# Performance work log

Measured on AMD Instinct MI355X. Metric: run time of the kernel, lower is better.

The kernel has to match this reference:

```python
import jax, jax.numpy as jnp
import numpy as np

D, E, DFF, TOPK = 768, 4, 1024, 2


def setup_inputs() -> dict:
    key = jax.random.key(0)
    ks = jax.random.split(key, 6)
    s = 0.02  # init scale for weights
    return {
        "input_ids": jax.random.normal(ks[0], (8, 2048, D), dtype=jnp.float32),
        "W": jax.random.normal(ks[1], (D, D), dtype=jnp.float32) * s,
        "b": jnp.zeros((D,), dtype=jnp.float32),
        "Wg": jax.random.normal(ks[2], (D, E), dtype=jnp.float32) * s,
        "bg": jnp.zeros((E,), dtype=jnp.float32),
        "W1": jax.random.normal(ks[3], (E, D, DFF), dtype=jnp.float32) * s,
        "b1": jnp.zeros((E, DFF), dtype=jnp.float32),
        "W2": jax.random.normal(ks[4], (E, DFF, D), dtype=jnp.float32) * s,
        "b2": jnp.zeros((E, D), dtype=jnp.float32),
    }


def reference(input_ids, W, b, Wg, bg, W1, b1, W2, b2):
    B, S, _ = input_ids.shape
    # Dense projection feeding the MoE layer
    h = jnp.einsum("bsd,de->bse", input_ids, W) + b          # [B,S,D]
    t = h.reshape(-1, D)                                      # [T,D] tokens

    # Token-choice router: softmax over experts, top-2, renormalized gates
    logits = t @ Wg + bg                                      # [T,E]
    probs = jax.nn.softmax(logits, axis=-1)
    vals, idx = jax.lax.top_k(probs, TOPK)                    # [T,K]
    gates = vals / jnp.sum(vals, axis=-1, keepdims=True)
    # Dense combine weights [T,E]: zero for non-selected experts
    comb = jnp.sum(jax.nn.one_hot(idx, E, dtype=t.dtype) * gates[..., None], axis=1)

    # Expert FFNs (E small -> compute all experts, weighted combine)
    pre = jnp.einsum("td,edf->etf", t, W1) + b1[:, None, :]   # [E,T,DFF]
    y_e = jnp.einsum("etf,efd->etd", jax.nn.gelu(pre), W2) + b2[:, None, :]
    out = jnp.einsum("te,etd->td", comb, y_e)                 # [T,D]
    return out.reshape(B, S, D)
```

## Files before the change

### kernel.cpp

```cpp
#include <hip/hip_runtime.h>

#define DIM 768
#define NEXP 4
#define DFF_ 1024
#define CAP 16384

typedef __attribute__((ext_vector_type(4))) float f32x4;
typedef __attribute__((ext_vector_type(8))) short s16x8;

__device__ __forceinline__ unsigned short f32_to_bf16(float f) {
  unsigned int u = __float_as_uint(f);
  unsigned int r = (u + 0x7FFFu + ((u >> 16) & 1u)) >> 16;
  return (unsigned short)r;
}
__device__ __forceinline__ float bf16_to_f32(unsigned short u) {
  return __uint_as_float(((unsigned int)u) << 16);
}
__device__ __forceinline__ unsigned lds_off(const void* p) {
  return (unsigned)(unsigned long long)(__attribute__((address_space(3))) const void*)p;
}

__global__ void pack_bf16_kernel(const float* __restrict__ in,
                                 unsigned short* __restrict__ out,
                                 int K, int C) {
  const int t = threadIdx.x;
  const int lane = t & 63;
  const int pb = blockIdx.x * 4 + (t >> 6);
  const int KT = K >> 5;
  const int n16 = pb / KT, kt = pb - n16 * KT;
  const int z = blockIdx.z;
  in  += (size_t)z * K * C;
  out += (size_t)z * K * C;
  const int col = n16 * 16 + (lane & 15);
  const int k0 = kt * 32 + (lane >> 4) * 8;
  s16x8 vv;
#pragma unroll
  for (int e = 0; e < 8; e++) vv[e] = (short)f32_to_bf16(in[(size_t)(k0 + e) * C + col]);
  *(s16x8*)(out + (size_t)pb * 512 + lane * 8) = vv;
}

__global__ void wfg_kernel(const float* __restrict__ W, const float* __restrict__ Wg,
                           const float* __restrict__ b, const float* __restrict__ bg,
                           float* __restrict__ wfg, float* __restrict__ bgp) {
  int gid = blockIdx.x * 256 + threadIdx.x;
  if (gid < DIM * NEXP) {
    int k = gid >> 2, e = gid & 3;
    const float* wr = W + (size_t)k * DIM;
    float acc = 0.f;
    for (int d = 0; d < DIM; d++) acc += wr[d] * Wg[d * NEXP + e];
    wfg[gid] = acc;
  } else if (gid < DIM * NEXP + NEXP) {
    int e = gid - DIM * NEXP;
    float acc = bg[e];
    for (int d = 0; d < DIM; d++) acc += b[d] * Wg[d * NEXP + e];
    bgp[e] = acc;
  }
}

__global__ void router_kernel(const float* __restrict__ x, const float* __restrict__ wfg,
                              const float* __restrict__ bgp,
                              int2* __restrict__ rte, float2* __restrict__ rtg,
                              unsigned short* __restrict__ xbf) {
  __shared__ float wfgS[DIM * NEXP];
  const int tid = threadIdx.x;
  for (int i = tid; i < DIM * NEXP; i += 256) wfgS[i] = wfg[i];
  __syncthreads();
  const int w = tid >> 6, lane = tid & 63;
  const size_t t = (size_t)blockIdx.x * 4 + w;
  const float* xr = x + t * DIM;
  unsigned short* xbr = xbf + t * DIM;
  float a0 = 0.f, a1 = 0.f, a2 = 0.f, a3 = 0.f;
#pragma unroll
  for (int i = 0; i < 6; i++) {
    int k = i * 128 + lane * 2;
    float2 xv = *(const float2*)(xr + k);
    ushort2 pk;
    pk.x = f32_to_bf16(xv.x);
    pk.y = f32_to_bf16(xv.y);
    *(ushort2*)(xbr + k) = pk;
    a0 += xv.x * wfgS[k * 4 + 0] + xv.y * wfgS[k * 4 + 4];
    a1 += xv.x * wfgS[k * 4 + 1] + xv.y * wfgS[k * 4 + 5];
    a2 += xv.x * wfgS[k * 4 + 2] + xv.y * wfgS[k * 4 + 6];
    a3 += xv.x * wfgS[k * 4 + 3] + xv.y * wfgS[k * 4 + 7];
  }
#pragma unroll
  for (int off = 32; off > 0; off >>= 1) {
    a0 += __shfl_xor(a0, off);
    a1 += __shfl_xor(a1, off);
    a2 += __shfl_xor(a2, off);
    a3 += __shfl_xor(a3, off);
  }
  if (lane == 0) {
    float l[NEXP] = {a0 + bgp[0], a1 + bgp[1], a2 + bgp[2], a3 + bgp[3]};
    float m = fmaxf(fmaxf(l[0], l[1]), fmaxf(l[2], l[3]));
    float p[NEXP]; float s = 0.f;
#pragma unroll
    for (int e = 0; e < NEXP; e++) { p[e] = expf(l[e] - m); s += p[e]; }
#pragma unroll
    for (int e = 0; e < NEXP; e++) p[e] /= s;
    int i1 = 0;
#pragma unroll
    for (int e = 1; e < NEXP; e++) if (p[e] > p[i1]) i1 = e;
    int i2 = -1;
#pragma unroll
    for (int e = 0; e < NEXP; e++) { if (e == i1) continue; if (i2 < 0 || p[e] > p[i2]) i2 = e; }
    float denom = p[i1] + p[i2];
    rte[t] = make_int2(i1, i2);
    rtg[t] = make_float2(p[i1] / denom, p[i2] / denom);
  }
}

__global__ void assign_kernel(const int2* __restrict__ rte, const float2* __restrict__ rtg,
                              int* __restrict__ cnt, int* __restrict__ idx_tok,
                              float* __restrict__ gate_sel, int2* __restrict__ tok_slot) {
  __shared__ int hist[NEXP];
  __shared__ int base[NEXP];
  const int tid = threadIdx.x;
  if (tid < NEXP) hist[tid] = 0;
  __syncthreads();
  const int t = blockIdx.x * 256 + tid;
  int2 e = rte[t];
  float2 g = rtg[t];
  int r1 = atomicAdd(&hist[e.x], 1);
  int r2 = atomicAdd(&hist[e.y], 1);
  __syncthreads();
  if (tid < NEXP) base[tid] = atomicAdd(&cnt[tid], hist[tid]);
  __syncthreads();
  int s1 = base[e.x] + r1, s2 = base[e.y] + r2;
  idx_tok[e.x * CAP + s1] = t;  gate_sel[e.x * CAP + s1] = g.x;
  idx_tok[e.y * CAP + s2] = t;  gate_sel[e.y * CAP + s2] = g.y;
  tok_slot[t] = make_int2((e.x << 14) | s1, (e.y << 14) | s2);
}

__global__ void combine_kernel(const unsigned short* __restrict__ y,
                               const int2* __restrict__ tok_slot,
                               const float2* __restrict__ rtg,
                               const int* __restrict__ cnts,
                               const float* __restrict__ b2,
                               float* __restrict__ out) {
  __shared__ float b2S[NEXP * DIM];
  const int tid = threadIdx.x;
  for (int i = tid; i < NEXP * DIM; i += 256) b2S[i] = b2[i];
  const int t0 = (cnts[0] + 127) >> 7, t1 = (cnts[1] + 127) >> 7, t2 = (cnts[2] + 127) >> 7;
  const int rb[NEXP] = {0, t0 * 128, (t0 + t1) * 128, (t0 + t1 + t2) * 128};
  __syncthreads();
  const int w = tid >> 6, lane = tid & 63;
  const size_t t = (size_t)blockIdx.x * 4 + w;
  int2 v = tok_slot[t];
  float2 cg = rtg[t];
  const int e1 = v.x >> 14, s1 = v.x & (CAP - 1);
  const int e2 = v.y >> 14, s2 = v.y & (CAP - 1);
  const unsigned short* y1 = y + (size_t)(rb[e1] + s1) * DIM;
  const unsigned short* y2 = y + (size_t)(rb[e2] + s2) * DIM;
  float* op = out + t * DIM;
  const float* bp1 = b2S + e1 * DIM;
  const float* bp2 = b2S + e2 * DIM;
#pragma unroll
  for (int k = 0; k < 12; k++) {
    int n = k * 64 + lane;
    op[n] = bf16_to_f32(y1[n]) + bf16_to_f32(y2[n]) + cg.x * bp1[n] + cg.y * bp2[n];
  }
}

template <int MODE, int CH, int NT>
__launch_bounds__(256, 3)
__global__ void gemm_kernel(const unsigned short* __restrict__ A, const int lda,
                            const unsigned short* __restrict__ Bp, const int ldb,
                            const int N,
                            const float* __restrict__ bias,
                            const int* __restrict__ idx_tok,
                            const float* __restrict__ gate_sel,
                            const int* __restrict__ cnts,
                            unsigned short* __restrict__ outB, const int ldo) {
  const int lin = blockIdx.y * gridDim.x + blockIdx.x;
  const int nT = gridDim.x;
  const int xcd = lin & 7, t8 = lin >> 3;
  int bn = 0, bm0 = 0;
  int bmLoc = 0, cnt = 1 << 30, segBase = 0, gRow0 = 0;
  const unsigned short* Bt = Bp;

  if constexpr (MODE == 0) {
    const int perXcd = gridDim.y >> 3;
    const int mi = t8 % CH;
    const int rest = t8 / CH;
    bn = rest % nT;
    const int mc = rest / nT;
    bm0 = (xcd * perXcd + mc * CH + mi) * 128;
  } else {
    const int c0 = cnts[0], c1 = cnts[1], c2 = cnts[2], c3 = cnts[3];
    const int t0 = (c0 + 127) >> 7, t1 = (c1 + 127) >> 7,
              t2 = (c2 + 127) >> 7, t3 = (c3 + 127) >> 7;
    const int p1 = t0, p2 = p1 + t1, p3 = p2 + t2, tot = p3 + t3;
    const int perXcd = (tot + 7) >> 3;
    bn = t8 % nT;
    const int mloc = t8 / nT;
    if (mloc >= perXcd) return;
    const int mIdx = xcd * perXcd + mloc;
    if (mIdx >= tot) return;
    const int seg = (mIdx >= p2) ? ((mIdx >= p3) ? 3 : 2) : ((mIdx >= p1) ? 1 : 0);
    const int pre = (seg == 3) ? p3 : (seg == 2) ? p2 : (seg == 1) ? p1 : 0;
    bmLoc = (mIdx - pre) * 128;
    segBase = seg * CAP;
    gRow0 = mIdx * 128;
    cnt = (seg == 3) ? c3 : (seg == 2) ? c2 : (seg == 1) ? c1 : c0;
    Bt += (size_t)seg * N * ldb;
    if constexpr (MODE == 1) bias += (size_t)seg * N;
  }

  __shared__ unsigned short As[4][3][2048];
  __shared__ int idxS[128];
  __shared__ float gateS[128];

  const int tid = threadIdx.x;
  const int w = tid >> 6;
  const int lane = tid & 63;

  if constexpr (MODE == 1) {
    if (tid < 128) {
      int r = bmLoc + tid;
      int cl = (r < cnt) ? r : bmLoc;
      idxS[tid] = idx_tok[segBase + cl];
      gateS[tid] = gate_sel[segBase + cl];
    }
    __syncthreads();
  }

  const int quad = lane >> 4;
  const int m16 = lane & 15;
  const int wm = (w & 1) * 64;
  const int wn = (w >> 1) * 64;

  const int lrow = lane >> 2;
  const int lslot = (lane & 3) ^ (lrow & 3);
  const unsigned short* aSrc[4];
#pragma unroll
  for (int q = 0; q < 4; q++) {
    const int rw = q * 16 + lrow;
    size_t grow;
    if constexpr (MODE == 0) grow = (size_t)(bm0 + wm + rw);
    else if constexpr (MODE == 1) grow = (size_t)idxS[wm + rw];
    else grow = (size_t)(gRow0 + wm + rw);
    aSrc[q] = A + grow * lda + lslot * 8;
  }

  const unsigned wBase = lds_off(&As[w][0][0]);
  const unsigned aRd = (unsigned)(m16 * 64 + ((quad ^ (m16 & 3)) * 16));
  const unsigned aAd0 = wBase + aRd;
  const unsigned aAd1 = wBase + 4096u + aRd;
  const unsigned aAd2 = wBase + 8192u + aRd;

  const unsigned short* bq0 = Bt + (size_t)(bn * 8 + (w >> 1) * 4 + 0) * NT * 512 + lane * 8;
  const unsigned short* bq1 = Bt + (size_t)(bn * 8 + (w >> 1) * 4 + 1) * NT * 512 + lane * 8;
  const unsigned short* bq2 = Bt + (size_t)(bn * 8 + (w >> 1) * 4 + 2) * NT * 512 + lane * 8;
  const unsigned short* bq3 = Bt + (size_t)(bn * 8 + (w >> 1) * 4 + 3) * NT * 512 + lane * 8;

  f32x4 acc[4][4];
#pragma unroll
  for (int i = 0; i < 4; i++)
#pragma unroll
    for (int j = 0; j < 4; j++) acc[i][j] = (f32x4){0.f, 0.f, 0.f, 0.f};

  s16x8 br[3][4];

#define GLL(src, dst)                                                              \
  __builtin_amdgcn_global_load_lds((const __attribute__((address_space(1))) void*)(src), \
                                   (__attribute__((address_space(3))) void*)(dst), 16, 0, 0)
#define GLLA(kt_)                                                        \
  {                                                                      \
    char* d_ = (char*)&As[w][(kt_) % 3][0];                              \
    GLL(aSrc[0] + (kt_) * 32, d_);                                       \
    GLL(aSrc[1] + (kt_) * 32, d_ + 1024);                                \
    GLL(aSrc[2] + (kt_) * 32, d_ + 2048);                                \
    GLL(aSrc[3] + (kt_) * 32, d_ + 3072);                                \
  }
#define LOADB(kt_)                                                                             \
  {                                                                                            \
    asm volatile("global_load_dwordx4 %0, %1, off" : "=v"(br[(kt_) % 3][0]) : "v"(bq0 + (kt_) * 512)); \
    asm volatile("global_load_dwordx4 %0, %1, off" : "=v"(br[(kt_) % 3][1]) : "v"(bq1 + (kt_) * 512)); \
    asm volatile("global_load_dwordx4 %0, %1, off" : "=v"(br[(kt_) % 3][2]) : "v"(bq2 + (kt_) * 512)); \
    asm volatile("global_load_dwordx4 %0, %1, off" : "=v"(br[(kt_) % 3][3]) : "v"(bq3 + (kt_) * 512)); \
  }
#define DSR(dst, addr, imm) \
  asm volatile("ds_read_b128 %0, %1 offset:" #imm : "=v"(dst) : "v"(addr))
#define KGATE(N) asm volatile("s_waitcnt vmcnt(" #N ")" ::: "memory")

  GLLA(0); LOADB(0);
  GLLA(1); LOADB(1);

  static_assert(NT >= 4, "NT must be >= 4");
#pragma unroll
  for (int kt = 0; kt < NT; ++kt) {
    if (kt + 2 < NT) { GLLA(kt + 2); LOADB(kt + 2); }
    if (kt < NT - 2) { KGATE(16); }
    else if (kt == NT - 2) { KGATE(8); }
    else { KGATE(0); }
    __builtin_amdgcn_sched_barrier(0);
    s16x8 af[4];
    const unsigned aAd = ((kt % 3) == 0) ? aAd0 : ((kt % 3) == 1) ? aAd1 : aAd2;
    DSR(af[0], aAd, 0);
    DSR(af[1], aAd, 1024);
    DSR(af[2], aAd, 2048);
    DSR(af[3], aAd, 3072);
    asm volatile("s_waitcnt lgkmcnt(0)" ::: "memory");
    __builtin_amdgcn_sched_barrier(0);
    __builtin_amdgcn_s_setprio(1);
#pragma unroll
    for (int i_ = 0; i_ < 4; i_++)
#pragma unroll
      for (int j_ = 0; j_ < 4; j_++)
        acc[i_][j_] = __builtin_amdgcn_mfma_f32_16x16x32_bf16(af[i_], br[kt % 3][j_],
                                                              acc[i_][j_], 0, 0, 0);
    __builtin_amdgcn_s_setprio(0);
  }

#undef KGATE
#undef DSR
#undef LOADB
#undef GLLA
#undef GLL

#pragma unroll
  for (int i = 0; i < 4; i++) {
    const int rloc = wm + i * 16 + quad * 4;
#pragma unroll
    for (int j = 0; j < 4; j++) {
      const int col = bn * 128 + wn + j * 16 + m16;
      if constexpr (MODE == 0) {
        float bv = bias[col];
#pragma unroll
        for (int r = 0; r < 4; r++)
          outB[(size_t)(bm0 + rloc + r) * ldo + col] = f32_to_bf16(acc[i][j][r] + bv);
      } else if constexpr (MODE == 1) {
        float bv = bias[col];
#pragma unroll
        for (int r = 0; r < 4; r++) {
          if (bmLoc + rloc + r < cnt) {
            float v = acc[i][j][r] + bv;
            float t3 = v + 0.044715f * v * v * v;
            float e2 = exp2f(t3 * 2.302208206984525f);
            float rc = __builtin_amdgcn_rcpf(1.0f + e2);
            float g = v - v * rc;
            outB[(size_t)(gRow0 + rloc + r) * ldo + col] = f32_to_bf16(g * gateS[rloc + r]);
          }
        }
      } else {
#pragma unroll
        for (int r = 0; r < 4; r++) {
          if (bmLoc + rloc + r < cnt)
            outB[(size_t)(gRow0 + rloc + r) * ldo + col] = f32_to_bf16(acc[i][j][r]);
        }
      }
    }
  }
}

extern "C" void kernel_launch(void* const* d_in, const int* in_sizes, int n_in,
                              void* d_out, int out_size, void* d_ws, size_t ws_size,
                              hipStream_t stream) {
  (void)in_sizes; (void)n_in; (void)out_size; (void)ws_size;
  const float* x  = (const float*)d_in[0];
  const float* W  = (const float*)d_in[1];
  const float* b  = (const float*)d_in[2];
  const float* Wg = (const float*)d_in[3];
  const float* bg = (const float*)d_in[4];
  const float* W1 = (const float*)d_in[5];
  const float* b1 = (const float*)d_in[6];
  const float* W2 = (const float*)d_in[7];
  const float* b2 = (const float*)d_in[8];
  float* out = (float*)d_out;
  char* ws = (char*)d_ws;

  unsigned short* tbf  = (unsigned short*)(ws + 0);
  unsigned short* w1p  = (unsigned short*)(ws + 25165824);
  unsigned short* w2p  = (unsigned short*)(ws + 31457280);
  float* wfg           = (float*)(ws + 37748736);
  float* bgp           = (float*)(ws + 37761024);
  int2*  rte           = (int2*)(ws + 37761280);
  float2* rtg          = (float2*)(ws + 37892352);
  int*   cnt           = (int*)(ws + 38023424);
  int*   idx_tok       = (int*)(ws + 38023680);
  float* gate_sel      = (float*)(ws + 38285824);
  int2*  tok_slot      = (int2*)(ws + 38547968);
  unsigned short* g    = (unsigned short*)(ws + 38679040);
  unsigned short* xbf  = (unsigned short*)(ws + 38679040);
  unsigned short* wp   = (unsigned short*)(ws + 63844864);
  unsigned short* y    = (unsigned short*)(ws + 106574336);

  hipMemsetAsync(cnt, 0, NEXP * sizeof(int), stream);
  pack_bf16_kernel<<<dim3(288, 1, 1), 256, 0, stream>>>(W, wp, 768, 768);
  pack_bf16_kernel<<<dim3(384, 1, 4), 256, 0, stream>>>(W1, w1p, 768, 1024);
  pack_bf16_kernel<<<dim3(384, 1, 4), 256, 0, stream>>>(W2, w2p, 1024, 768);
  wfg_kernel<<<13, 256, 0, stream>>>(W, Wg, b, bg, wfg, bgp);
  router_kernel<<<4096, 256, 0, stream>>>(x, wfg, bgp, rte, rtg, xbf);
  assign_kernel<<<64, 256, 0, stream>>>(rte, rtg, cnt, idx_tok, gate_sel, tok_slot);

  gemm_kernel<0, 8, 24><<<dim3(6, 128), 256, 0, stream>>>(
      xbf, 768, wp, 768, 768, b, nullptr, nullptr, nullptr, tbf, 768);
  gemm_kernel<1, 8, 24><<<dim3(8, 264), 256, 0, stream>>>(
      tbf, 768, w1p, 768, 1024, b1, idx_tok, gate_sel, cnt, g, 1024);
  gemm_kernel<2, 8, 32><<<dim3(6, 264), 256, 0, stream>>>(
      g, 1024, w2p, 1024, 768, nullptr, nullptr, nullptr, cnt, y, 768);
  combine_kernel<<<4096, 256, 0, stream>>>(y, tok_slot, rtg, cnt, b2, out);
}
```

Before: 412.0 us.

## Load A fragments directly into registers, dropping LDS staging

New measurement: 513.4 us. +24.6%, slower.

```diff
diff --git a/kernel.cpp b/kernel.cpp
--- a/kernel.cpp
+++ b/kernel.cpp
@@ -15,9 +15,6 @@
 }
 __device__ __forceinline__ float bf16_to_f32(unsigned short u) {
   return __uint_as_float(((unsigned int)u) << 16);
-}
-__device__ __forceinline__ unsigned lds_off(const void* p) {
-  return (unsigned)(unsigned long long)(__attribute__((address_space(3))) const void*)p;
 }
 
 __global__ void pack_bf16_kernel(const float* __restrict__ in,
@@ -207,7 +204,6 @@
     if constexpr (MODE == 1) bias += (size_t)seg * N;
   }
 
-  __shared__ unsigned short As[4][3][2048];
   __shared__ int idxS[128];
   __shared__ float gateS[128];
 
@@ -230,29 +226,21 @@
   const int wm = (w & 1) * 64;
   const int wn = (w >> 1) * 64;
 
-  const int lrow = lane >> 2;
-  const int lslot = (lane & 3) ^ (lrow & 3);
-  const unsigned short* aSrc[4];
-#pragma unroll
-  for (int q = 0; q < 4; q++) {
-    const int rw = q * 16 + lrow;
+  const unsigned short* aq[4];
+#pragma unroll
+  for (int i = 0; i < 4; i++) {
+    const int rl = wm + i * 16 + m16;
     size_t grow;
-    if constexpr (MODE == 0) grow = (size_t)(bm0 + wm + rw);
-    else if constexpr (MODE == 1) grow = (size_t)idxS[wm + rw];
-    else grow = (size_t)(gRow0 + wm + rw);
-    aSrc[q] = A + grow * lda + lslot * 8;
-  }
-
-  const unsigned wBase = lds_off(&As[w][0][0]);
-  const unsigned aRd = (unsigned)(m16 * 64 + ((quad ^ (m16 & 3)) * 16));
-  const unsigned aAd0 = wBase + aRd;
-  const unsigned aAd1 = wBase + 4096u + aRd;
-  const unsigned aAd2 = wBase + 8192u + aRd;
-
-  const unsigned short* bq0 = Bt + (size_t)(bn * 8 + (w >> 1) * 4 + 0) * NT * 512 + lane * 8;
-  const unsigned short* bq1 = Bt + (size_t)(bn * 8 + (w >> 1) * 4 + 1) * NT * 512 + lane * 8;
-  const unsigned short* bq2 = Bt + (size_t)(bn * 8 + (w >> 1) * 4 + 2) * NT * 512 + lane * 8;
-  const unsigned short* bq3 = Bt + (size_t)(bn * 8 + (w >> 1) * 4 + 3) * NT * 512 + lane * 8;
+    if constexpr (MODE == 0) grow = (size_t)(bm0 + rl);
+    else if constexpr (MODE == 1) grow = (size_t)idxS[rl];
+    else grow = (size_t)(gRow0 + rl);
+    aq[i] = A + grow * lda + quad * 8;
+  }
+
+  const unsigned short* bq[4];
+#pragma unroll
+  for (int j = 0; j < 4; j++)
+    bq[j] = Bt + (size_t)(bn * 8 + (w >> 1) * 4 + j) * NT * 512 + lane * 8;
 
   f32x4 acc[4][4];
 #pragma unroll
@@ -260,64 +248,52 @@
 #pragma unroll
     for (int j = 0; j < 4; j++) acc[i][j] = (f32x4){0.f, 0.f, 0.f, 0.f};
 
-  s16x8 br[3][4];
-
-#define GLL(src, dst)                                                              \
-  __builtin_amdgcn_global_load_lds((const __attribute__((address_space(1))) void*)(src), \
-                                   (__attribute__((address_space(3))) void*)(dst), 16, 0, 0)
-#define GLLA(kt_)                                                        \
+  s16x8 ar[2][4], br[2][4];
+
+#define LOADA(kt_)                                                       \
   {                                                                      \
-    char* d_ = (char*)&As[w][(kt_) % 3][0];                              \
-    GLL(aSrc[0] + (kt_) * 32, d_);                                       \
-    GLL(aSrc[1] + (kt_) * 32, d_ + 1024);                                \
-    GLL(aSrc[2] + (kt_) * 32, d_ + 2048);                                \
-    GLL(aSrc[3] + (kt_) * 32, d_ + 3072);                                \
-  }
-#define LOADB(kt_)                                                                             \
-  {                                                                                            \
-    asm volatile("global_load_dwordx4 %0, %1, off" : "=v"(br[(kt_) % 3][0]) : "v"(bq0 + (kt_) * 512)); \
-    asm volatile("global_load_dwordx4 %0, %1, off" : "=v"(br[(kt_) % 3][1]) : "v"(bq1 + (kt_) * 512)); \
-    asm volatile("global_load_dwordx4 %0, %1, off" : "=v"(br[(kt_) % 3][2]) : "v"(bq2 + (kt_) * 512)); \
-    asm volatile("global_load_dwordx4 %0, %1, off" : "=v"(br[(kt_) % 3][3]) : "v"(bq3 + (kt_) * 512)); \
-  }
-#define DSR(dst, addr, imm) \
-  asm volatile("ds_read_b128 %0, %1 offset:" #imm : "=v"(dst) : "v"(addr))
+    _Pragma("unroll") for (int i_ = 0; i_ < 4; i_++) {                   \
+      asm volatile("global_load_dwordx4 %0, %1, off"                     \
+                   : "=v"(ar[(kt_) & 1][i_]) : "v"(aq[i_]));             \
+    }                                                                    \
+  }
+#define LOADB(kt_)                                                       \
+  {                                                                      \
+    _Pragma("unroll") for (int j_ = 0; j_ < 4; j_++) {                   \
+      asm volatile("global_load_dwordx4 %0, %1, off"                     \
+                   : "=v"(br[(kt_) & 1][j_]) : "v"(bq[j_]));             \
+    }                                                                    \
+  }
+#define ADV()                                                            \
+  {                                                                      \
+    _Pragma("unroll") for (int i_ = 0; i_ < 4; i_++) aq[i_] += 32;       \
+    _Pragma("unroll") for (int j_ = 0; j_ < 4; j_++) bq[j_] += 512;      \
+  }
 #define KGATE(N) asm volatile("s_waitcnt vmcnt(" #N ")" ::: "memory")
 
-  GLLA(0); LOADB(0);
-  GLLA(1); LOADB(1);
-
-  static_assert(NT >= 4, "NT must be >= 4");
+  LOADA(0); LOADB(0); ADV();
+
+  static_assert(NT >= 2, "NT must be >= 2");
 #pragma unroll
   for (int kt = 0; kt < NT; ++kt) {
-    if (kt + 2 < NT) { GLLA(kt + 2); LOADB(kt + 2); }
-    if (kt < NT - 2) { KGATE(16); }
-    else if (kt == NT - 2) { KGATE(8); }
-    else { KGATE(0); }
-    __builtin_amdgcn_sched_barrier(0);
-    s16x8 af[4];
-    const unsigned aAd = ((kt % 3) == 0) ? aAd0 : ((kt % 3) == 1) ? aAd1 : aAd2;
-    DSR(af[0], aAd, 0);
-    DSR(af[1], aAd, 1024);
-    DSR(af[2], aAd, 2048);
-    DSR(af[3], aAd, 3072);
-    asm volatile("s_waitcnt lgkmcnt(0)" ::: "memory");
+    if (kt + 1 < NT) { LOADA(kt + 1); LOADB(kt + 1); ADV(); }
+    if (kt < NT - 1) { KGATE(8); }
+    else            { KGATE(0); }
     __builtin_amdgcn_sched_barrier(0);
     __builtin_amdgcn_s_setprio(1);
 #pragma unroll
     for (int i_ = 0; i_ < 4; i_++)
 #pragma unroll
       for (int j_ = 0; j_ < 4; j_++)
-        acc[i_][j_] = __builtin_amdgcn_mfma_f32_16x16x32_bf16(af[i_], br[kt % 3][j_],
+        acc[i_][j_] = __builtin_amdgcn_mfma_f32_16x16x32_bf16(ar[kt & 1][i_], br[kt & 1][j_],
                                                               acc[i_][j_], 0, 0, 0);
     __builtin_amdgcn_s_setprio(0);
   }
 
 #undef KGATE
-#undef DSR
+#undef ADV
 #undef LOADB
-#undef GLLA
-#undef GLL
+#undef LOADA
 
 #pragma unroll
   for (int i = 0; i < 4; i++) {
```
